# Kernel tuning notes

Hardware: AMD Instinct MI355X
Metric: run time of the kernel (lower is better)

Reference implementation:

```python
import jax, jax.numpy as jnp
import numpy as np
from jax import lax

DIM = 192
PATCH = 8


def conv1x1(x, w):
    # x: [b,c,h,w], w: [o,c] (1x1 conv, no bias)
    return jnp.einsum('bchw,oc->bohw', x, w)


def dwconv(x, w, b, pad):
    # depthwise conv, w: [C,1,kh,kw], groups = C
    y = lax.conv_general_dilated(
        x, w, window_strides=(1, 1), padding=((pad, pad), (pad, pad)),
        dimension_numbers=('NCHW', 'OIHW', 'NCHW'),
        feature_group_count=x.shape[1])
    return y + b[None, :, None, None]


def to_patches(x, p):
    b, c, h, w = x.shape
    ph = (-h) % p
    pw = (-w) % p
    x = jnp.pad(x, ((0, 0), (0, 0), (0, ph), (0, pw)))
    H, W = h + ph, w + pw
    x = x.reshape(b, c, H // p, p, W // p, p)
    return x.transpose(0, 1, 2, 4, 3, 5)  # b c nh nw p p


def from_patches(x, h, w):
    b, c, nh, nw, p, _ = x.shape
    x = x.transpose(0, 1, 2, 4, 3, 5).reshape(b, c, nh * p, nw * p)
    return x[:, :, :h, :w]


def setup_inputs() -> dict:
    key = jax.random.key(0)
    ks = jax.random.split(key, 8)
    b, c, h, w = 4, DIM, 256, 256
    x = jax.random.normal(ks[0], (b, c, h, w), jnp.float32)
    wq = jax.random.normal(ks[1], (c, c), jnp.float32) * 0.02
    w_qdw = jax.random.normal(ks[2], (c, 1, 3, 3), jnp.float32) * 0.1
    b_qdw = jnp.zeros((c,), jnp.float32)
    wkv = jax.random.normal(ks[3], (2 * c, c), jnp.float32) * 0.02
    w_kvdw = jax.random.normal(ks[4], (2 * c, 1, 7, 7), jnp.float32) * 0.05
    b_kvdw = jnp.zeros((2 * c,), jnp.float32)
    ln_w = jnp.ones((c,), jnp.float32)
    ln_b = jnp.zeros((c,), jnp.float32)
    w_proj = jax.random.normal(ks[5], (c, c), jnp.float32) * 0.02
    b_proj = jnp.zeros((c,), jnp.float32)
    return {'x': x, 'wq': wq, 'w_qdw': w_qdw, 'b_qdw': b_qdw,
            'wkv': wkv, 'w_kvdw': w_kvdw, 'b_kvdw': b_kvdw,
            'ln_w': ln_w, 'ln_b': ln_b, 'w_proj': w_proj, 'b_proj': b_proj}


def reference(x, wq, w_qdw, b_qdw, wkv, w_kvdw, b_kvdw, ln_w, ln_b, w_proj, b_proj):
    b, c, h, w = x.shape
    p = PATCH
    q = dwconv(conv1x1(x, wq), w_qdw, b_qdw, pad=1)
    kv = dwconv(conv1x1(x, wkv), w_kvdw, b_kvdw, pad=3)
    k, v = kv[:, :c], kv[:, c:]
    qp = to_patches(q, p).astype(jnp.float32)
    kp = to_patches(k, p).astype(jnp.float32)
    out = jnp.fft.irfft2(jnp.fft.rfft2(qp) * jnp.fft.rfft2(kp), s=(p, p))
    out = from_patches(out, h, w)
    # WithBias LayerNorm over channel dim (channels-last LN in original)
    mu = out.mean(axis=1, keepdims=True)
    var = out.var(axis=1, keepdims=True)
    out = (out - mu) / jnp.sqrt(var + 1e-5)
    out = out * ln_w[None, :, None, None] + ln_b[None, :, None, None]
    out = out * v
    out = conv1x1(out, w_proj) + b_proj[None, :, None, None]
    return out
```

## Files before the change

### kernel.cpp

```cpp
#include <hip/hip_runtime.h>
#include <hip/hip_bf16.h>

#define HW 65536
#define IMG 256
static constexpr int CDIM = 192;

typedef __attribute__((ext_vector_type(8))) short short8;
typedef __attribute__((ext_vector_type(4))) short s16x4;
typedef __attribute__((ext_vector_type(4))) float f32x4;
typedef __attribute__((ext_vector_type(2))) float f32x2;

static constexpr size_t BS_X   = (size_t)CDIM * HW;
static constexpr size_t BS_XT  = (size_t)HW * 192;
static constexpr size_t BS_QKV = (size_t)576 * HW;
static constexpr size_t BS_KV  = (size_t)384 * HW;
static constexpr size_t BS_S   = (size_t)192 * HW;
static constexpr size_t BS_OUT = (size_t)192 * HW;

static __device__ __forceinline__ float b2f(unsigned short u) {
    union { unsigned u; float f; } t; t.u = ((unsigned)u) << 16; return t.f;
}
static __device__ __forceinline__ unsigned short f2bu(float f) {
    __hip_bfloat16 h = __float2bfloat16(f);
    return *reinterpret_cast<unsigned short*>(&h);
}

__global__ void pack_weights(const float* __restrict__ wq,
                             const float* __restrict__ wkv,
                             const float* __restrict__ wp,
                             __hip_bfloat16* __restrict__ Wqkv,
                             __hip_bfloat16* __restrict__ Wp) {
    int i = blockIdx.x * 256 + threadIdx.x;
    if (i < 36864) Wqkv[i] = __float2bfloat16(wq[i]);
    else if (i < 110592) Wqkv[i] = __float2bfloat16(wkv[i - 36864]);
    else if (i < 147456) Wp[i - 110592] = __float2bfloat16(wp[i - 110592]);
}

__global__ void transpose_cvt(const float* __restrict__ x,
                              __hip_bfloat16* __restrict__ xT) {
    __shared__ float tile[32][33];
    x  += (size_t)blockIdx.z * BS_X;
    xT += (size_t)blockIdx.z * BS_XT;
    const int p0 = blockIdx.x * 32, c0 = blockIdx.y * 32;
    const int tx = threadIdx.x & 31, ty = threadIdx.x >> 5;
#pragma unroll
    for (int r = 0; r < 4; r++)
        tile[ty + r * 8][tx] = x[(size_t)(c0 + ty + r * 8) * HW + p0 + tx];
    __syncthreads();
    const int pl = threadIdx.x >> 3, cl = (threadIdx.x & 7) * 4;
    union { unsigned short h[4]; unsigned long long u; } ob;
#pragma unroll
    for (int e = 0; e < 4; e++) ob.h[e] = f2bu(tile[cl + e][pl]);
    *(unsigned long long*)(xT + (size_t)(p0 + pl) * 192 + c0 + cl) = ob.u;
}

__global__ void gemm_bf16(const __hip_bfloat16* __restrict__ A,
                          const __hip_bfloat16* __restrict__ Bt,
                          __hip_bfloat16* __restrict__ Y) {
    __shared__ short Bs[64][200];
    Bt += (size_t)blockIdx.z * BS_XT;
    Y  += (size_t)blockIdx.z * BS_QKV;
    const int tid = threadIdx.x;
    const int wid = tid >> 6, lane = tid & 63;
    const int mBase = blockIdx.x * 64, nBase = blockIdx.y * 64;

#pragma unroll
    for (int l = 0; l < 6; l++) {
        int ch = tid + l * 256;
        int row = ch / 24, cc = ch % 24;
        short8 v = *(const short8*)(Bt + (size_t)(nBase + row) * 192 + cc * 8);
        *(short8*)&Bs[row][cc * 8] = v;
    }
    __syncthreads();

    const int lr = lane & 15, lg = lane >> 4;
    const __hip_bfloat16* Ab = A + (size_t)(mBase + wid * 16 + lr) * 192 + lg * 8;
    f32x4 acc[4];
#pragma unroll
    for (int f = 0; f < 4; f++) acc[f] = (f32x4){0.f, 0.f, 0.f, 0.f};

#pragma unroll
    for (int ks = 0; ks < 6; ks++) {
        short8 af = *(const short8*)(Ab + ks * 32);
#pragma unroll
        for (int f = 0; f < 4; f++) {
            short8 bfr = *(const short8*)&Bs[f * 16 + lr][ks * 32 + lg * 8];
            acc[f] = __builtin_amdgcn_mfma_f32_16x16x32_bf16(af, bfr, acc[f], 0, 0, 0);
        }
    }

    const int mrow = mBase + wid * 16 + lg * 4;
#pragma unroll
    for (int f = 0; f < 4; f++) {
        int n = nBase + f * 16 + lr;
#pragma unroll
        for (int r = 0; r < 4; r++)
            Y[(size_t)(mrow + r) * HW + n] = __float2bfloat16(acc[f][r]);
    }
}

__global__ __launch_bounds__(256) void dwconv7_v8(
    const __hip_bfloat16* __restrict__ in,
    const float* __restrict__ wdw,
    const float* __restrict__ bias,
    __hip_bfloat16* __restrict__ out) {
    __shared__ unsigned short tile[70][136];
    in  += (size_t)blockIdx.z * BS_QKV;
    out += (size_t)blockIdx.z * BS_KV;
    const int c = blockIdx.y;
    const int x0 = blockIdx.x * 128;
    const __hip_bfloat16* src = in + (size_t)c * HW;

    float w49[49];
#pragma unroll
    for (int i = 0; i < 49; i++) w49[i] = wdw[c * 49 + i];
    const float bval = bias[c];

    const int tid = threadIdx.x;
    short8 pre[5];

    auto load_tasks = [&](int t) {
#pragma unroll
        for (int l = 0; l < 5; l++) {
            int idx = tid + l * 256;
            short8 v = (short8){0, 0, 0, 0, 0, 0, 0, 0};
            if (idx < 70 * 17) {
                int r = idx / 17, cs = idx - r * 17;
                int gy = t * 64 + r - 3;
                int gxb = x0 + cs * 8 - 3;
                if ((unsigned)gy < IMG && gxb >= 0 && gxb + 8 <= IMG) {
                    v = *(const short8*)(src + gy * IMG + gxb);
                } else if ((unsigned)gy < IMG) {
#pragma unroll
                    for (int e = 0; e < 8; e++) {
                        int gx = gxb + e;
                        if ((unsigned)gx < IMG)
                            v[e] = *(const short*)(src + gy * IMG + gx);
                    }
                }
            }
            pre[l] = v;
        }
    };

    load_tasks(0);

    const int tx4 = (tid & 31) * 4;
    const int gy8 = (tid >> 5) * 8;

    for (int t = 0; t < 4; t++) {
        __syncthreads();
#pragma unroll
        for (int l = 0; l < 5; l++) {
            int idx = tid + l * 256;
            if (idx < 70 * 17) {
                int r = idx / 17, cs = idx - r * 17;
                *(short8*)&tile[r][cs * 8] = pre[l];
            }
        }
        __syncthreads();
        if (t < 3) load_tasks(t + 1);

        f32x2 acc2[8][2];
#pragma unroll
        for (int j = 0; j < 8; j++) {
            acc2[j][0] = (f32x2){bval, bval};
            acc2[j][1] = (f32x2){bval, bval};
        }

#pragma unroll
        for (int rr = 0; rr < 14; rr++) {
            const unsigned short* rowp = &tile[gy8 + rr][tx4];
            s16x4 a0 = *(const s16x4*)(rowp);
            s16x4 a1 = *(const s16x4*)(rowp + 4);
            s16x4 a2 = *(const s16x4*)(rowp + 8);
            float win[12];
#pragma unroll
            for (int e = 0; e < 4; e++) {
                win[e]     = b2f((unsigned short)a0[e]);
                win[e + 4] = b2f((unsigned short)a1[e]);
                win[e + 8] = b2f((unsigned short)a2[e]);
            }
#pragma unroll
            for (int j = 0; j < 8; j++) {
                const int ky = rr - j;
                if (ky >= 0 && ky < 7) {
#pragma unroll
                    for (int kx = 0; kx < 7; kx++) {
                        const float w = w49[ky * 7 + kx];
                        const f32x2 wv = (f32x2){w, w};
                        acc2[j][0] += (f32x2){win[kx], win[kx + 1]} * wv;
                        acc2[j][1] += (f32x2){win[kx + 2], win[kx + 3]} * wv;
                    }
                }
            }
        }

        __hip_bfloat16* dst = out + (size_t)c * HW +
                              (size_t)(t * 64 + gy8) * IMG + x0 + tx4;
#pragma unroll
        for (int j = 0; j < 8; j++) {
            union { unsigned short h[4]; unsigned long long u; } ob;
            ob.h[0] = f2bu(acc2[j][0][0]);
            ob.h[1] = f2bu(acc2[j][0][1]);
            ob.h[2] = f2bu(acc2[j][1][0]);
            ob.h[3] = f2bu(acc2[j][1][1]);
            *(unsigned long long*)(dst + (size_t)j * IMG) = ob.u;
        }
    }
}

__global__ __launch_bounds__(256) void circ_qfused(
    const __hip_bfloat16* __restrict__ q0,
    const __hip_bfloat16* __restrict__ kbuf,
    const float* __restrict__ w_qdw, const float* __restrict__ b_qdw,
    __hip_bfloat16* __restrict__ sout) {
    __shared__ float qs[10][264];
    __shared__ float qP[32][68];
    __shared__ float kP[32][68];
    q0   += (size_t)blockIdx.z * BS_QKV;
    kbuf += (size_t)blockIdx.z * BS_KV;
    sout += (size_t)blockIdx.z * BS_S;
    const int c = blockIdx.y, ph = blockIdx.x;
    const int y0 = ph * 8;
    const __hip_bfloat16* qsrc = q0 + (size_t)c * HW;
    const __hip_bfloat16* ksrc = kbuf + (size_t)c * HW;

    for (int t = threadIdx.x; t < 340; t += 256) {
        if (t < 320) {
            int r = t >> 5, ch = t & 31;
            int gy = y0 + r - 1;
            f32x4 lo = (f32x4){0.f, 0.f, 0.f, 0.f};
            f32x4 hi = (f32x4){0.f, 0.f, 0.f, 0.f};
            if ((unsigned)gy < IMG) {
                short8 v = *(const short8*)(qsrc + gy * IMG + ch * 8);
#pragma unroll
                for (int e = 0; e < 4; e++) {
                    lo[e] = b2f((unsigned short)v[e]);
                    hi[e] = b2f((unsigned short)v[4 + e]);
                }
            }
            *(f32x4*)&qs[r][4 + ch * 8] = lo;
            *(f32x4*)&qs[r][8 + ch * 8] = hi;
        } else {
            int e = t - 320;
            int r = e >> 1, s = e & 1;
            qs[r][s ? 260 : 3] = 0.f;
        }
    }
    {
        int a = threadIdx.x >> 5, ch = threadIdx.x & 31;
        short8 v = *(const short8*)(ksrc + (y0 + a) * IMG + ch * 8);
        f32x4 lo, hi;
#pragma unroll
        for (int e = 0; e < 4; e++) {
            lo[e] = b2f((unsigned short)v[e]);
            hi[e] = b2f((unsigned short)v[4 + e]);
        }
        *(f32x4*)&kP[ch][a * 8] = lo;
        *(f32x4*)&kP[ch][a * 8 + 4] = hi;
    }
    __syncthreads();

    {
        const int x = threadIdx.x;
        float w9[9];
#pragma unroll
        for (int i = 0; i < 9; i++) w9[i] = w_qdw[c * 9 + i];
        float accq[8];
#pragma unroll
        for (int j = 0; j < 8; j++) accq[j] = b_qdw[c];
#pragma unroll
        for (int kx = 0; kx < 3; kx++)
#pragma unroll
            for (int yy = 0; yy < 10; yy++) {
                float vv = qs[yy][x + kx + 3];
#pragma unroll
                for (int j = 0; j < 8; j++) {
                    int ky = yy - j;
                    if (ky >= 0 && ky < 3) accq[j] += vv * w9[ky * 3 + kx];
                }
            }
#pragma unroll
        for (int j = 0; j < 8; j++) qP[x >> 3][j * 8 + (x & 7)] = accq[j];
    }
    __syncthreads();

    const int i = threadIdx.x >> 5, pw = threadIdx.x & 31;
    float qv[8][8];
#pragma unroll
    for (int a = 0; a < 8; a++) {
        f32x4 u0 = *(const f32x4*)&qP[pw][a * 8];
        f32x4 u1 = *(const f32x4*)&qP[pw][a * 8 + 4];
        qv[a][0] = u0[0]; qv[a][1] = u0[1]; qv[a][2] = u0[2]; qv[a][3] = u0[3];
        qv[a][4] = u1[0]; qv[a][5] = u1[1]; qv[a][6] = u1[2]; qv[a][7] = u1[3];
    }
    f32x2 acc2[4];
#pragma unroll
    for (int j2 = 0; j2 < 4; j2++) acc2[j2] = (f32x2){0.f, 0.f};

#pragma unroll
    for (int a = 0; a < 8; a++) {
        const int r = (i - a + 8) & 7;
        f32x4 k0v = *(const f32x4*)&kP[pw][r * 8];
        f32x4 k1v = *(const f32x4*)&kP[pw][r * 8 + 4];
        const float kr[8] = {k0v[0], k0v[1], k0v[2], k0v[3],
                             k1v[0], k1v[1], k1v[2], k1v[3]};
        const f32x2 krE[4] = {(f32x2){kr[0], kr[1]}, (f32x2){kr[2], kr[3]},
                              (f32x2){kr[4], kr[5]}, (f32x2){kr[6], kr[7]}};
        const f32x2 krS[4] = {(f32x2){kr[1], kr[2]}, (f32x2){kr[3], kr[4]},
                              (f32x2){kr[5], kr[6]}, (f32x2){kr[7], kr[0]}};
#pragma unroll
        for (int b = 0; b < 8; b += 2) {
            const float qe = qv[a][b];
            const float qo = qv[a][b + 1];
#pragma unroll
            for (int j2 = 0; j2 < 4; j2++) {
                const int re = (2 * j2 - b + 8) & 7;
                acc2[j2] += (f32x2){qe, qe} * krE[re >> 1];
                const int ro = (2 * j2 - b - 1 + 16) & 7;
                acc2[j2] += (f32x2){qo, qo} * krS[(ro - 1) >> 1];
            }
        }
    }
    union { unsigned short h[8]; short8 s8; } ob;
#pragma unroll
    for (int j = 0; j < 8; j++) ob.h[j] = f2bu(acc2[j >> 1][j & 1]);
    *(short8*)(sout + (size_t)c * HW + (size_t)(y0 + i) * IMG + pw * 8) = ob.s8;
}

__global__ __launch_bounds__(256, 2) void gemm_proj_ln(
    const __hip_bfloat16* __restrict__ Wp,
    const __hip_bfloat16* __restrict__ s,
    const __hip_bfloat16* __restrict__ v,
    const float* __restrict__ ln_w, const float* __restrict__ ln_b,
    const float* __restrict__ bias,
    float* __restrict__ Y) {
    __shared__ short Bs[128][200];
    __shared__ float red[2][2][128];
    __shared__ float muA[128], rsA[128];
    s += (size_t)blockIdx.z * BS_S;
    v += (size_t)blockIdx.z * BS_KV;
    Y += (size_t)blockIdx.z * BS_OUT;
    const int tid = threadIdx.x;
    const int p0 = blockIdx.x * 128;
    const int px = tid & 127, h = tid >> 7;
    const unsigned short* sp = (const unsigned short*)s;

    float sum = 0.f, sq = 0.f;
#pragma unroll 4
    for (int l = 0; l < 48; l++) {
        int c = h * 96 + l * 2;
        unsigned short ua = sp[(size_t)c * HW + p0 + px];
        unsigned short ub = sp[(size_t)(c + 1) * HW + p0 + px];
        float a = b2f(ua), b = b2f(ub);
        sum += a + b;
        sq += a * a + b * b;
        *(unsigned*)&Bs[px][c] = (unsigned)ua | ((unsigned)ub << 16);
    }
    red[h][0][px] = sum;
    red[h][1][px] = sq;
    __syncthreads();
    if (tid < 128) {
        float sm = red[0][0][tid] + red[1][0][tid];
        float sQ = red[0][1][tid] + red[1][1][tid];
        float mu = sm * (1.f / 192.f);
        float var = sQ * (1.f / 192.f) - mu * mu;
        muA[tid] = mu;
        rsA[tid] = rsqrtf(var + 1e-5f);
    }
    __syncthreads();

    const float mu = muA[px], rs = rsA[px];
#pragma unroll 4
    for (int l = 0; l < 48; l++) {
        int c = h * 96 + l * 2;
        unsigned pr = *(unsigned*)&Bs[px][c];
        float a = b2f((unsigned short)pr);
        float b = b2f((unsigned short)(pr >> 16));
        float va = b2f(*(const unsigned short*)(v + (size_t)c * HW + p0 + px));
        float vb = b2f(*(const unsigned short*)(v + (size_t)(c + 1) * HW + p0 + px));
        a = ((a - mu) * rs * ln_w[c] + ln_b[c]) * va;
        b = ((b - mu) * rs * ln_w[c + 1] + ln_b[c + 1]) * vb;
        *(unsigned*)&Bs[px][c] = (unsigned)f2bu(a) | ((unsigned)f2bu(b) << 16);
    }
    __syncthreads();

    const int wid = tid >> 6, lane = tid & 63;
    const int lr = lane & 15, lg = lane >> 4;
    f32x4 acc[3][8];
#pragma unroll
    for (int mf = 0; mf < 3; mf++)
#pragma unroll
        for (int f = 0; f < 8; f++) acc[mf][f] = (f32x4){0.f, 0.f, 0.f, 0.f};

#pragma unroll
    for (int ks = 0; ks < 6; ks++) {
        short8 bfr[8];
#pragma unroll
        for (int f = 0; f < 8; f++)
            bfr[f] = *(const short8*)&Bs[f * 16 + lr][ks * 32 + lg * 8];
#pragma unroll
        for (int mf = 0; mf < 3; mf++) {
            int mrow = wid * 48 + mf * 16 + lr;
            short8 af = *(const short8*)(Wp + (size_t)mrow * 192 + ks * 32 + lg * 8);
#pragma unroll
            for (int f = 0; f < 8; f++)
                acc[mf][f] = __builtin_amdgcn_mfma_f32_16x16x32_bf16(af, bfr[f], acc[mf][f], 0, 0, 0);
        }
    }

#pragma unroll
    for (int mf = 0; mf < 3; mf++) {
        int m0 = wid * 48 + mf * 16 + lg * 4;
#pragma unroll
        for (int f = 0; f < 8; f++) {
            int n = p0 + f * 16 + lr;
#pragma unroll
            for (int r = 0; r < 4; r++)
                Y[(size_t)(m0 + r) * HW + n] = acc[mf][f][r] + bias[m0 + r];
        }
    }
}

extern "C" void kernel_launch(void* const* d_in, const int* in_sizes, int n_in,
                              void* d_out, int out_size, void* d_ws, size_t ws_size,
                              hipStream_t stream) {
    const float* x      = (const float*)d_in[0];
    const float* wq     = (const float*)d_in[1];
    const float* w_qdw  = (const float*)d_in[2];
    const float* b_qdw  = (const float*)d_in[3];
    const float* wkv    = (const float*)d_in[4];
    const float* w_kvdw = (const float*)d_in[5];
    const float* b_kvdw = (const float*)d_in[6];
    const float* ln_w   = (const float*)d_in[7];
    const float* ln_b   = (const float*)d_in[8];
    const float* w_proj = (const float*)d_in[9];
    const float* b_proj = (const float*)d_in[10];
    float* out = (float*)d_out;
    char* ws = (char*)d_ws;

    __hip_bfloat16* qkv0  = (__hip_bfloat16*)(ws + 0);
    __hip_bfloat16* kvbuf = (__hip_bfloat16*)(ws + 150994944ull);
    __hip_bfloat16* sbuf  = (__hip_bfloat16*)(ws + 251658240ull);
    __hip_bfloat16* xT    = (__hip_bfloat16*)(ws + 301989888ull);
    __hip_bfloat16* Wqkv  = (__hip_bfloat16*)(ws + 352321536ull);
    __hip_bfloat16* Wp    = Wqkv + 110592;

    pack_weights<<<576, 256, 0, stream>>>(wq, wkv, w_proj, Wqkv, Wp);

    for (int p = 0; p < 2; p++) {
        const float* xp = x + (size_t)(p * 2) * BS_X;
        float* outp = out + (size_t)(p * 2) * BS_OUT;
        transpose_cvt<<<dim3(HW / 32, 6, 2), 256, 0, stream>>>(xp, xT);
        gemm_bf16<<<dim3(9, HW / 64, 2), 256, 0, stream>>>(Wqkv, xT, qkv0);
        dwconv7_v8<<<dim3(2, 384, 2), 256, 0, stream>>>(qkv0 + (size_t)192 * HW,
                                                        w_kvdw, b_kvdw, kvbuf);
        circ_qfused<<<dim3(32, 192, 2), 256, 0, stream>>>(qkv0, kvbuf,
                                                          w_qdw, b_qdw, sbuf);
        gemm_proj_ln<<<dim3(HW / 128, 1, 2), 256, 0, stream>>>(
            Wp, sbuf, kvbuf + (size_t)192 * HW, ln_w, ln_b, b_proj, outp);
    }
}
```

Before: 638.2 us.

## Process four patch rows per block with register-prefetched next tile

Each circ_qfused block now handles four consecutive 8-row patch strips instead of one, so the grid shrinks by four. The global loads for the next strip go into registers while the current strip's depthwise conv and circular convolution run. Depthwise weights and bias are loaded once per block, and global latency is meant to overlap with compute. The cost is fewer blocks, less parallelism, and more register pressure from the prefetched short8 values.

Result: no change. 637.9 us (median of 2 runs) (-0.0%).

```diff
diff --git a/kernel.cpp b/kernel.cpp
--- a/kernel.cpp
+++ b/kernel.cpp
@@ -221,112 +221,140 @@
     q0   += (size_t)blockIdx.z * BS_QKV;
     kbuf += (size_t)blockIdx.z * BS_KV;
     sout += (size_t)blockIdx.z * BS_S;
-    const int c = blockIdx.y, ph = blockIdx.x;
-    const int y0 = ph * 8;
+    const int c = blockIdx.y;
+    const int ph0 = blockIdx.x * 4;
     const __hip_bfloat16* qsrc = q0 + (size_t)c * HW;
     const __hip_bfloat16* ksrc = kbuf + (size_t)c * HW;
-
-    for (int t = threadIdx.x; t < 340; t += 256) {
-        if (t < 320) {
-            int r = t >> 5, ch = t & 31;
-            int gy = y0 + r - 1;
-            f32x4 lo = (f32x4){0.f, 0.f, 0.f, 0.f};
-            f32x4 hi = (f32x4){0.f, 0.f, 0.f, 0.f};
-            if ((unsigned)gy < IMG) {
-                short8 v = *(const short8*)(qsrc + gy * IMG + ch * 8);
+    const int tid = threadIdx.x;
+
+    float w9[9];
+#pragma unroll
+    for (int i = 0; i < 9; i++) w9[i] = w_qdw[c * 9 + i];
+    const float bq = b_qdw[c];
+
+    short8 pq[2], pk;
+    auto load_tile = [&](int t) {
+        const int y0 = (ph0 + t) * 8;
+#pragma unroll
+        for (int l = 0; l < 2; l++) {
+            int idx = tid + l * 256;
+            short8 v = (short8){0, 0, 0, 0, 0, 0, 0, 0};
+            if (idx < 320) {
+                int r = idx >> 5, ch = idx & 31;
+                int gy = y0 + r - 1;
+                if ((unsigned)gy < IMG)
+                    v = *(const short8*)(qsrc + gy * IMG + ch * 8);
+            }
+            pq[l] = v;
+        }
+        {
+            int a = tid >> 5, ch = tid & 31;
+            pk = *(const short8*)(ksrc + (y0 + a) * IMG + ch * 8);
+        }
+    };
+
+    load_tile(0);
+
+    const int i = tid >> 5, pw = tid & 31;
+
+    for (int t = 0; t < 4; t++) {
+        const int y0 = (ph0 + t) * 8;
+        __syncthreads();
+#pragma unroll
+        for (int l = 0; l < 2; l++) {
+            int idx = tid + l * 256;
+            if (idx < 320) {
+                int r = idx >> 5, ch = idx & 31;
+                f32x4 lo, hi;
 #pragma unroll
                 for (int e = 0; e < 4; e++) {
-                    lo[e] = b2f((unsigned short)v[e]);
-                    hi[e] = b2f((unsigned short)v[4 + e]);
+                    lo[e] = b2f((unsigned short)pq[l][e]);
+                    hi[e] = b2f((unsigned short)pq[l][4 + e]);
                 }
-            }
-            *(f32x4*)&qs[r][4 + ch * 8] = lo;
-            *(f32x4*)&qs[r][8 + ch * 8] = hi;
-        } else {
-            int e = t - 320;
-            int r = e >> 1, s = e & 1;
-            qs[r][s ? 260 : 3] = 0.f;
-        }
-    }
-    {
-        int a = threadIdx.x >> 5, ch = threadIdx.x & 31;
-        short8 v = *(const short8*)(ksrc + (y0 + a) * IMG + ch * 8);
-        f32x4 lo, hi;
-#pragma unroll
-        for (int e = 0; e < 4; e++) {
-            lo[e] = b2f((unsigned short)v[e]);
-            hi[e] = b2f((unsigned short)v[4 + e]);
-        }
-        *(f32x4*)&kP[ch][a * 8] = lo;
-        *(f32x4*)&kP[ch][a * 8 + 4] = hi;
-    }
-    __syncthreads();
-
-    {
-        const int x = threadIdx.x;
-        float w9[9];
-#pragma unroll
-        for (int i = 0; i < 9; i++) w9[i] = w_qdw[c * 9 + i];
-        float accq[8];
-#pragma unroll
-        for (int j = 0; j < 8; j++) accq[j] = b_qdw[c];
-#pragma unroll
-        for (int kx = 0; kx < 3; kx++)
-#pragma unroll
-            for (int yy = 0; yy < 10; yy++) {
-                float vv = qs[yy][x + kx + 3];
-#pragma unroll
-                for (int j = 0; j < 8; j++) {
-                    int ky = yy - j;
-                    if (ky >= 0 && ky < 3) accq[j] += vv * w9[ky * 3 + kx];
+                *(f32x4*)&qs[r][4 + ch * 8] = lo;
+                *(f32x4*)&qs[r][8 + ch * 8] = hi;
+            }
+        }
+        if (tid < 20) {
+            int r = tid >> 1, s2 = tid & 1;
+            qs[r][s2 ? 260 : 3] = 0.f;
+        }
+        {
+            int a = tid >> 5, ch = tid & 31;
+            f32x4 lo, hi;
+#pragma unroll
+            for (int e = 0; e < 4; e++) {
+                lo[e] = b2f((unsigned short)pk[e]);
+                hi[e] = b2f((unsigned short)pk[4 + e]);
+            }
+            *(f32x4*)&kP[ch][a * 8] = lo;
+            *(f32x4*)&kP[ch][a * 8 + 4] = hi;
+        }
+        __syncthreads();
+        if (t < 3) load_tile(t + 1);
+
+        {
+            const int x = tid;
+            float accq[8];
+#pragma unroll
+            for (int j = 0; j < 8; j++) accq[j] = bq;
+#pragma unroll
+            for (int kx = 0; kx < 3; kx++)
+#pragma unroll
+                for (int yy = 0; yy < 10; yy++) {
+                    float vv = qs[yy][x + kx + 3];
+#pragma unroll
+                    for (int j = 0; j < 8; j++) {
+                        int ky = yy - j;
+                        if (ky >= 0 && ky < 3) accq[j] += vv * w9[ky * 3 + kx];
+                    }
                 }
-            }
-#pragma unroll
-        for (int j = 0; j < 8; j++) qP[x >> 3][j * 8 + (x & 7)] = accq[j];
-    }
-    __syncthreads();
-
-    const int i = threadIdx.x >> 5, pw = threadIdx.x & 31;
-    float qv[8][8];
-#pragma unroll
-    for (int a = 0; a < 8; a++) {
-        f32x4 u0 = *(const f32x4*)&qP[pw][a * 8];
-        f32x4 u1 = *(const f32x4*)&qP[pw][a * 8 + 4];
-        qv[a][0] = u0[0]; qv[a][1] = u0[1]; qv[a][2] = u0[2]; qv[a][3] = u0[3];
-        qv[a][4] = u1[0]; qv[a][5] = u1[1]; qv[a][6] = u1[2]; qv[a][7] = u1[3];
-    }
-    f32x2 acc2[4];
-#pragma unroll
-    for (int j2 = 0; j2 < 4; j2++) acc2[j2] = (f32x2){0.f, 0.f};
-
-#pragma unroll
-    for (int a = 0; a < 8; a++) {
-        const int r = (i - a + 8) & 7;
-        f32x4 k0v = *(const f32x4*)&kP[pw][r * 8];
-        f32x4 k1v = *(const f32x4*)&kP[pw][r * 8 + 4];
-        const float kr[8] = {k0v[0], k0v[1], k0v[2], k0v[3],
-                             k1v[0], k1v[1], k1v[2], k1v[3]};
-        const f32x2 krE[4] = {(f32x2){kr[0], kr[1]}, (f32x2){kr[2], kr[3]},
-                              (f32x2){kr[4], kr[5]}, (f32x2){kr[6], kr[7]}};
-        const f32x2 krS[4] = {(f32x2){kr[1], kr[2]}, (f32x2){kr[3], kr[4]},
-                              (f32x2){kr[5], kr[6]}, (f32x2){kr[7], kr[0]}};
-#pragma unroll
-        for (int b = 0; b < 8; b += 2) {
-            const float qe = qv[a][b];
-            const float qo = qv[a][b + 1];
-#pragma unroll
-            for (int j2 = 0; j2 < 4; j2++) {
-                const int re = (2 * j2 - b + 8) & 7;
-                acc2[j2] += (f32x2){qe, qe} * krE[re >> 1];
-                const int ro = (2 * j2 - b - 1 + 16) & 7;
-                acc2[j2] += (f32x2){qo, qo} * krS[(ro - 1) >> 1];
-            }
-        }
-    }
-    union { unsigned short h[8]; short8 s8; } ob;
-#pragma unroll
-    for (int j = 0; j < 8; j++) ob.h[j] = f2bu(acc2[j >> 1][j & 1]);
-    *(short8*)(sout + (size_t)c * HW + (size_t)(y0 + i) * IMG + pw * 8) = ob.s8;
+#pragma unroll
+            for (int j = 0; j < 8; j++) qP[x >> 3][j * 8 + (x & 7)] = accq[j];
+        }
+        __syncthreads();
+
+        float qv[8][8];
+#pragma unroll
+        for (int a = 0; a < 8; a++) {
+            f32x4 u0 = *(const f32x4*)&qP[pw][a * 8];
+            f32x4 u1 = *(const f32x4*)&qP[pw][a * 8 + 4];
+            qv[a][0] = u0[0]; qv[a][1] = u0[1]; qv[a][2] = u0[2]; qv[a][3] = u0[3];
+            qv[a][4] = u1[0]; qv[a][5] = u1[1]; qv[a][6] = u1[2]; qv[a][7] = u1[3];
+        }
+        f32x2 acc2[4];
+#pragma unroll
+        for (int j2 = 0; j2 < 4; j2++) acc2[j2] = (f32x2){0.f, 0.f};
+
+#pragma unroll
+        for (int a = 0; a < 8; a++) {
+            const int r = (i - a + 8) & 7;
+            f32x4 k0v = *(const f32x4*)&kP[pw][r * 8];
+            f32x4 k1v = *(const f32x4*)&kP[pw][r * 8 + 4];
+            const float kr[8] = {k0v[0], k0v[1], k0v[2], k0v[3],
+                                 k1v[0], k1v[1], k1v[2], k1v[3]};
+            const f32x2 krE[4] = {(f32x2){kr[0], kr[1]}, (f32x2){kr[2], kr[3]},
+                                  (f32x2){kr[4], kr[5]}, (f32x2){kr[6], kr[7]}};
+            const f32x2 krS[4] = {(f32x2){kr[1], kr[2]}, (f32x2){kr[3], kr[4]},
+                                  (f32x2){kr[5], kr[6]}, (f32x2){kr[7], kr[0]}};
+#pragma unroll
+            for (int b = 0; b < 8; b += 2) {
+                const float qe = qv[a][b];
+                const float qo = qv[a][b + 1];
+#pragma unroll
+                for (int j2 = 0; j2 < 4; j2++) {
+                    const int re = (2 * j2 - b + 8) & 7;
+                    acc2[j2] += (f32x2){qe, qe} * krE[re >> 1];
+                    const int ro = (2 * j2 - b - 1 + 16) & 7;
+                    acc2[j2] += (f32x2){qo, qo} * krS[(ro - 1) >> 1];
+                }
+            }
+        }
+        union { unsigned short h[8]; short8 s8; } ob;
+#pragma unroll
+        for (int j = 0; j < 8; j++) ob.h[j] = f2bu(acc2[j >> 1][j & 1]);
+        *(short8*)(sout + (size_t)c * HW + (size_t)(y0 + i) * IMG + pw * 8) = ob.s8;
+    }
 }
 
 __global__ __launch_bounds__(256, 2) void gemm_proj_ln(
@@ -456,8 +484,8 @@
         gemm_bf16<<<dim3(9, HW / 64, 2), 256, 0, stream>>>(Wqkv, xT, qkv0);
         dwconv7_v8<<<dim3(2, 384, 2), 256, 0, stream>>>(qkv0 + (size_t)192 * HW,
                                                         w_kvdw, b_kvdw, kvbuf);
-        circ_qfused<<<dim3(32, 192, 2), 256, 0, stream>>>(qkv0, kvbuf,
-                                                          w_qdw, b_qdw, sbuf);
+        circ_qfused<<<dim3(8, 192, 2), 256, 0, stream>>>(qkv0, kvbuf,
+                                                         w_qdw, b_qdw, sbuf);
         gemm_proj_ln<<<dim3(HW / 128, 1, 2), 256, 0, stream>>>(
             Wp, sbuf, kvbuf + (size_t)192 * HW, ln_w, ln_b, b_proj, outp);
     }
```
